# Kernel tuning notes

Measured on AMD Instinct MI355X. Metric: run time of the kernel, lower is better.

Reference implementation:

```python
import jax, jax.numpy as jnp
import numpy as np

N_NODES = 100000
N_EDGES = 1600000
IN_FEAT = 256
HIDDEN = 64
N_CLASSES = 16


def gcn_conv(x, edge_index, W, b):
    """PyG GCNConv: add self-loops, symmetric normalization, linear+aggregate."""
    n = x.shape[0]
    src, dst = edge_index[0], edge_index[1]
    loops = jnp.arange(n, dtype=src.dtype)
    src = jnp.concatenate([src, loops])
    dst = jnp.concatenate([dst, loops])
    # in-degree on graph with self-loops
    deg = jax.ops.segment_sum(jnp.ones(src.shape[0], dtype=x.dtype), dst, num_segments=n)
    dinv = jnp.where(deg > 0, jax.lax.rsqrt(deg), 0.0)
    h = x @ W                                  # [N, out]
    norm = dinv[src] * dinv[dst]               # [E+N]
    msg = h[src] * norm[:, None]                # gather + scale (memory-bound)
    out = jax.ops.segment_sum(msg, dst, num_segments=n)  # scatter-add
    return out + b


def setup_inputs() -> dict:
    key = jax.random.key(0)
    ks = jax.random.split(key, 5)
    x = jax.random.normal(ks[0], (N_NODES, IN_FEAT), dtype=jnp.float32)
    edge_index = jax.random.randint(ks[1], (2, N_EDGES), 0, N_NODES, dtype=jnp.int64)
    W1 = jax.random.normal(ks[2], (IN_FEAT, HIDDEN), dtype=jnp.float32) * (1.0 / np.sqrt(IN_FEAT))
    b1 = jnp.zeros((HIDDEN,), dtype=jnp.float32)
    W2 = jax.random.normal(ks[3], (HIDDEN, N_CLASSES), dtype=jnp.float32) * (1.0 / np.sqrt(HIDDEN))
    b2 = jnp.zeros((N_CLASSES,), dtype=jnp.float32)
    return {"x": x, "edge_index": edge_index, "W1": W1, "b1": b1, "W2": W2, "b2": b2}


def reference(x, edge_index, W1, b1, W2, b2):
    h = gcn_conv(x, edge_index, W1, b1)
    h = jax.nn.relu(h)
    # dropout p=0.5 is identity in eval mode (training=False)
    out = gcn_conv(h, edge_index, W2, b2)
    return out
```

## Files before the change

### kernel.cpp

```cpp
#include <hip/hip_runtime.h>

#define NN 100000
#define NE 1600000
#define FIN 256
#define FH 64
#define FC 16

#define NPB 512
#define NBKT ((NN + NPB - 1) / NPB)
#define NBLK 256
#define CHUNK (NE / NBLK)
#define CAP 12288
#define NB_GEMM1 ((NN + 127) / 128)

typedef int v2i __attribute__((ext_vector_type(2)));
typedef int v4i __attribute__((ext_vector_type(4)));
typedef short s16x8 __attribute__((ext_vector_type(8)));
typedef float f32x4 __attribute__((ext_vector_type(4)));

__device__ __forceinline__ float4 fma4(float4 v, float w, float4 a) {
    a.x = fmaf(v.x, w, a.x); a.y = fmaf(v.y, w, a.y);
    a.z = fmaf(v.z, w, a.z); a.w = fmaf(v.w, w, a.w);
    return a;
}
__device__ __forceinline__ float4 add4(float4 a, float4 v) {
    a.x += v.x; a.y += v.y; a.z += v.z; a.w += v.w;
    return a;
}
__device__ __forceinline__ float4 xor_add4(float4 r, int m) {
    r.x += __shfl_xor(r.x, m, 64); r.y += __shfl_xor(r.y, m, 64);
    r.z += __shfl_xor(r.z, m, 64); r.w += __shfl_xor(r.w, m, 64);
    return r;
}

__device__ __forceinline__ unsigned short bf16rne(float f) {
    unsigned u = __float_as_uint(f);
    u += 0x7FFFu + ((u >> 16) & 1u);
    return (unsigned short)(u >> 16);
}
__device__ __forceinline__ void split8(const float* f, s16x8& hi, s16x8& lo) {
    #pragma unroll
    for (int i = 0; i < 8; i++) {
        unsigned u = __float_as_uint(f[i]);
        unsigned short h = (unsigned short)((u + 0x7FFFu + ((u >> 16) & 1u)) >> 16);
        float l = f[i] - __uint_as_float((unsigned)h << 16);
        unsigned ul = __float_as_uint(l);
        hi[i] = (short)h;
        lo[i] = (short)((ul + 0x7FFFu + ((ul >> 16) & 1u)) >> 16);
    }
}

__global__ __launch_bounds__(256) void prep_k(const int* __restrict__ ei,
                                              int* __restrict__ flag,
                                              const float* __restrict__ W,
                                              unsigned short* __restrict__ Whi,
                                              unsigned short* __restrict__ Wlo) {
    int b = blockIdx.x;
    if (b == 8) {
        if (threadIdx.x == 0) {
            int z = (ei[1] == 0) & (ei[3] == 0) & (ei[5] == 0) & (ei[7] == 0);
            *flag = z;
        }
        return;
    }
    int slot = b * 256 + threadIdx.x;
    int l = slot & 63;
    int c = (slot >> 6) & 3;
    int s = slot >> 8;
    int k0 = s * 32 + (l >> 4) * 8;
    int col = c * 16 + (l & 15);
    #pragma unroll
    for (int i = 0; i < 8; i++) {
        float f = W[(k0 + i) * FH + col];
        unsigned short h = bf16rne(f);
        float lres = f - __uint_as_float((unsigned)h << 16);
        Whi[slot * 8 + i] = h;
        Wlo[slot * 8 + i] = bf16rne(lres);
    }
}

__global__ __launch_bounds__(256, 4) void gemm1_k(const float* __restrict__ x,
                                                  const unsigned short* __restrict__ Whi,
                                                  const unsigned short* __restrict__ Wlo,
                                                  float* __restrict__ h1) {
    const int t = threadIdx.x;
    const int lane = t & 63;
    const int wid = t >> 6;
    const int mb = blockIdx.x * 128 + wid * 32;
    const int lr = lane & 15;
    const int lk = (lane >> 4) * 8;

    int ra0 = mb + lr;
    int ra1 = mb + 16 + lr;
    const float* pa0 = x + (size_t)(ra0 < NN ? ra0 : NN - 1) * FIN + lk;
    const float* pa1 = x + (size_t)(ra1 < NN ? ra1 : NN - 1) * FIN + lk;

    f32x4 acc[2][4] = {};

    for (int s = 0; s < 8; s++) {
        float fa0[8], fa1[8];
        float4 q;
        q = *(const float4*)(pa0 + s * 32);
        fa0[0] = q.x; fa0[1] = q.y; fa0[2] = q.z; fa0[3] = q.w;
        q = *(const float4*)(pa0 + s * 32 + 4);
        fa0[4] = q.x; fa0[5] = q.y; fa0[6] = q.z; fa0[7] = q.w;
        q = *(const float4*)(pa1 + s * 32);
        fa1[0] = q.x; fa1[1] = q.y; fa1[2] = q.z; fa1[3] = q.w;
        q = *(const float4*)(pa1 + s * 32 + 4);
        fa1[4] = q.x; fa1[5] = q.y; fa1[6] = q.z; fa1[7] = q.w;

        s16x8 a0h, a0l, a1h, a1l;
        split8(fa0, a0h, a0l);
        split8(fa1, a1h, a1l);

        #pragma unroll
        for (int c = 0; c < 4; c++) {
            s16x8 wh = *(const s16x8*)&Whi[((s * 4 + c) * 64 + lane) * 8];
            s16x8 wl = *(const s16x8*)&Wlo[((s * 4 + c) * 64 + lane) * 8];
            acc[0][c] = __builtin_amdgcn_mfma_f32_16x16x32_bf16(a0h, wh, acc[0][c], 0, 0, 0);
            acc[0][c] = __builtin_amdgcn_mfma_f32_16x16x32_bf16(a0l, wh, acc[0][c], 0, 0, 0);
            acc[0][c] = __builtin_amdgcn_mfma_f32_16x16x32_bf16(a0h, wl, acc[0][c], 0, 0, 0);
            acc[1][c] = __builtin_amdgcn_mfma_f32_16x16x32_bf16(a1h, wh, acc[1][c], 0, 0, 0);
            acc[1][c] = __builtin_amdgcn_mfma_f32_16x16x32_bf16(a1l, wh, acc[1][c], 0, 0, 0);
            acc[1][c] = __builtin_amdgcn_mfma_f32_16x16x32_bf16(a1h, wl, acc[1][c], 0, 0, 0);
        }
    }
    #pragma unroll
    for (int r = 0; r < 2; r++) {
        int rowb = mb + 16 * r + (lane >> 4) * 4;
        #pragma unroll
        for (int c = 0; c < 4; c++) {
            #pragma unroll
            for (int v = 0; v < 4; v++) {
                int row = rowb + v;
                if (row < NN)
                    h1[(size_t)row * FH + 16 * c + lr] = acc[r][c][v];
            }
        }
    }
}

__global__ __launch_bounds__(256) void hist_k(const int* __restrict__ ei,
                                              const int* __restrict__ flag,
                                              int* __restrict__ cnt) {
    __shared__ int hist[NBKT];
    const int t = threadIdx.x, blk = blockIdx.x;
    for (int j = t; j < NBKT; j += 256) hist[j] = 0;
    __syncthreads();
    int f = *flag;
    int base = blk * CHUNK;
    if (f) {
        for (int i = t; i < CHUNK; i += 256) {
            v2i p = *(const v2i*)&ei[2 * (NE + base + i)];
            atomicAdd(&hist[p.x >> 9], 1);
        }
    } else {
        for (int i = t; i < CHUNK; i += 256) {
            int d = ei[NE + base + i];
            atomicAdd(&hist[d >> 9], 1);
        }
    }
    __syncthreads();
    for (int j = t; j < NBKT; j += 256) cnt[j * NBLK + blk] = hist[j];
}

__global__ __launch_bounds__(1024) void scanoff_k(int* __restrict__ cnt,
                                                  int* __restrict__ bucketBase) {
    __shared__ int s[1024];
    const int t = threadIdx.x;
    const int SEG = (NBKT * NBLK) / 1024;
    int base = t * SEG;
    int sum = 0;
    for (int i = 0; i < SEG; i++) sum += cnt[base + i];
    s[t] = sum; __syncthreads();
    for (int off = 1; off < 1024; off <<= 1) {
        int u = (t >= off) ? s[t - off] : 0;
        __syncthreads();
        s[t] += u;
        __syncthreads();
    }
    int run = s[t] - sum;
    for (int i = 0; i < SEG; i++) {
        int g = base + i;
        int v = cnt[g];
        cnt[g] = run;
        if ((g & (NBLK - 1)) == 0) bucketBase[g / NBLK] = run;
        run += v;
    }
    if (t == 0) bucketBase[NBKT] = NE;
}

__global__ __launch_bounds__(256) void scat_k(const int* __restrict__ ei,
                                              const int* __restrict__ flag,
                                              const int* __restrict__ cnt,
                                              int* __restrict__ sorted) {
    __shared__ int offl[NBKT];
    const int t = threadIdx.x, blk = blockIdx.x;
    for (int j = t; j < NBKT; j += 256) offl[j] = cnt[j * NBLK + blk];
    __syncthreads();
    int f = *flag;
    int base = blk * CHUNK;
    if (f) {
        for (int i = t; i < CHUNK; i += 256) {
            int e = base + i;
            v2i ps = *(const v2i*)&ei[2 * e];
            v2i pd = *(const v2i*)&ei[2 * (NE + e)];
            int s = ps.x, d = pd.x;
            int pos = atomicAdd(&offl[d >> 9], 1);
            sorted[pos] = s | ((d & (NPB - 1)) << 17);
        }
    } else {
        for (int i = t; i < CHUNK; i += 256) {
            int e = base + i;
            int s = ei[e], d = ei[NE + e];
            int pos = atomicAdd(&offl[d >> 9], 1);
            sorted[pos] = s | ((d & (NPB - 1)) << 17);
        }
    }
}

__global__ __launch_bounds__(256) void bucket_k(const int* __restrict__ sorted,
                                                const int* __restrict__ bucketBase,
                                                int* __restrict__ csr,
                                                int* __restrict__ row_start,
                                                float* __restrict__ dinv,
                                                float* __restrict__ h1) {
    __shared__ int stash[CAP];
    __shared__ int hist[NPB];
    __shared__ int startl[NPB];
    __shared__ int cursor[NPB];
    __shared__ int ss[256];
    const int t = threadIdx.x, b = blockIdx.x;
    const int nb0 = b * NPB;
    const int ncnt = (NN - nb0 < NPB) ? (NN - nb0) : NPB;
    const int ebase = bucketBase[b];
    const int ecnt = bucketBase[b + 1] - ebase;

    hist[t] = 0; hist[t + 256] = 0;
    __syncthreads();
    for (int i = t; i < ecnt; i += 256) {
        int v = sorted[ebase + i];
        if (i < CAP) stash[i] = v;
        atomicAdd(&hist[v >> 17], 1);
    }
    __syncthreads();
    int a = hist[2 * t], c = hist[2 * t + 1];
    int p = a + c;
    ss[t] = p; __syncthreads();
    for (int off = 1; off < 256; off <<= 1) {
        int u = (t >= off) ? ss[t - off] : 0;
        __syncthreads();
        ss[t] += u;
        __syncthreads();
    }
    int ex = ss[t] - p;
    startl[2 * t] = ex;       startl[2 * t + 1] = ex + a;
    cursor[2 * t] = ex;       cursor[2 * t + 1] = ex + a;
    __syncthreads();
    for (int j = t; j < ncnt; j += 256) {
        row_start[nb0 + j] = ebase + startl[j];
        dinv[nb0 + j] = rsqrtf((float)(hist[j] + 1));
    }
    if (b == 0 && t == 0) row_start[NN] = NE;
    for (int i = t; i < ecnt; i += 256) {
        int v = (i < CAP) ? stash[i] : sorted[ebase + i];
        int dl = v >> 17;
        int r = atomicAdd(&cursor[dl], 1);
        csr[ebase + r] = v & 0x1FFFF;
    }
    for (int q = t; q < ncnt * 16; q += 256) {
        int rl = q >> 4;
        float dv = rsqrtf((float)(hist[rl] + 1));
        size_t off = (size_t)(nb0 + rl) * FH + (q & 15) * 4;
        float4 v = *(const float4*)&h1[off];
        v.x *= dv; v.y *= dv; v.z *= dv; v.w *= dv;
        *(float4*)&h1[off] = v;
    }
}

__global__ __launch_bounds__(256) void agg1g_k(const int* __restrict__ csr,
                                               const int* __restrict__ row_start,
                                               const float* __restrict__ h1,
                                               const float* __restrict__ dinv,
                                               const float* __restrict__ b1,
                                               const float* __restrict__ W2,
                                               float* __restrict__ h2) {
    __shared__ float sW2[FH * FC];
    __shared__ float sp[4][FH];
    const int t = threadIdx.x;
    #pragma unroll
    for (int i = 0; i < 4; i++) sW2[t + 256 * i] = W2[t + 256 * i];
    __syncthreads();

    int wid = t >> 6;
    int n = blockIdx.x * 4 + wid;
    int lane = t & 63;
    if (n >= NN) return;
    int sg = lane >> 4;
    int fl = lane & 15;
    int s0 = row_start[n], s1 = row_start[n + 1];
    float4 A = make_float4(0.f, 0.f, 0.f, 0.f);
    float4 B = make_float4(0.f, 0.f, 0.f, 0.f);
    float4 C = make_float4(0.f, 0.f, 0.f, 0.f);
    float4 D = make_float4(0.f, 0.f, 0.f, 0.f);
    for (int j0 = s0; j0 < s1; j0 += 64) {
        int idx = j0 + lane;
        int sl = (idx < s1) ? csr[idx] : 0;
        int cnt = s1 - j0; if (cnt > 64) cnt = 64;
        int j = 0;
        for (; j + 16 <= cnt; j += 16) {
            int eA = __shfl(sl, j + sg, 64);
            int eB = __shfl(sl, j + 4 + sg, 64);
            int eC = __shfl(sl, j + 8 + sg, 64);
            int eD = __shfl(sl, j + 12 + sg, 64);
            float4 vA = *(const float4*)&h1[eA * FH + fl * 4];
            float4 vB = *(const float4*)&h1[eB * FH + fl * 4];
            float4 vC = *(const float4*)&h1[eC * FH + fl * 4];
            float4 vD = *(const float4*)&h1[eD * FH + fl * 4];
            A = add4(A, vA); B = add4(B, vB);
            C = add4(C, vC); D = add4(D, vD);
        }
        if (j + 8 <= cnt) {
            int eA = __shfl(sl, j + sg, 64);
            int eB = __shfl(sl, j + 4 + sg, 64);
            float4 vA = *(const float4*)&h1[eA * FH + fl * 4];
            float4 vB = *(const float4*)&h1[eB * FH + fl * 4];
            A = add4(A, vA); B = add4(B, vB);
            j += 8;
        }
        if (j + 4 <= cnt) {
            int eA = __shfl(sl, j + sg, 64);
            float4 vA = *(const float4*)&h1[eA * FH + fl * 4];
            A = add4(A, vA);
            j += 4;
        }
        int rem = cnt - j;
        if (rem > 0) {
            int jj = j + (sg < rem ? sg : 0);
            int eA = __shfl(sl, jj, 64);
            float wA = (sg < rem) ? 1.f : 0.f;
            float4 vA = *(const float4*)&h1[eA * FH + fl * 4];
            A = fma4(vA, wA, A);
        }
    }
    float4 r = add4(add4(A, B), add4(C, D));
    r = xor_add4(r, 16);
    r = xor_add4(r, 32);
    float dn = dinv[n];
    if (sg == 0) {
        float4 self = *(const float4*)&h1[n * FH + fl * 4];
        float4 bq = *(const float4*)&b1[fl * 4];
        float4 p;
        p.x = fmaxf(fmaf(r.x + self.x, dn, bq.x), 0.f);
        p.y = fmaxf(fmaf(r.y + self.y, dn, bq.y), 0.f);
        p.z = fmaxf(fmaf(r.z + self.z, dn, bq.z), 0.f);
        p.w = fmaxf(fmaf(r.w + self.w, dn, bq.w), 0.f);
        *(float4*)&sp[wid][fl * 4] = p;
    }
    __builtin_amdgcn_s_waitcnt(0);
    if (lane < FC) {
        float o = 0.f;
        #pragma unroll 8
        for (int k = 0; k < FH; k++)
            o = fmaf(sp[wid][k], sW2[k * FC + lane], o);
        h2[n * FC + lane] = o * dn;
    }
}

__global__ __launch_bounds__(256) void agg2_k(const int* __restrict__ csr,
                                              const int* __restrict__ row_start,
                                              const float* __restrict__ h2,
                                              const float* __restrict__ dinv,
                                              const float* __restrict__ b2,
                                              float* __restrict__ out) {
    const int t = threadIdx.x;
    int n = blockIdx.x * 16 + (t >> 4);
    int l16 = t & 15;
    int base = t & 48;
    int q = (t >> 2) & 3;
    int c = t & 3;
    if (n >= NN) return;
    int s0 = row_start[n], s1 = row_start[n + 1];
    float4 A = make_float4(0.f, 0.f, 0.f, 0.f);
    float4 B = make_float4(0.f, 0.f, 0.f, 0.f);
    float4 C = make_float4(0.f, 0.f, 0.f, 0.f);
    float4 D = make_float4(0.f, 0.f, 0.f, 0.f);
    for (int j0 = s0; j0 < s1; j0 += 16) {
        int idx = j0 + l16;
        int sl = (idx < s1) ? csr[idx] : 0;
        int cnt = s1 - j0; if (cnt > 16) cnt = 16;
        int j = 0;
        if (j + 16 <= cnt) {
            int eA = __shfl(sl, base + j + q, 64);
            int eB = __shfl(sl, base + j + 4 + q, 64);
            int eC = __shfl(sl, base + j + 8 + q, 64);
            int eD = __shfl(sl, base + j + 12 + q, 64);
            float4 vA = *(const float4*)&h2[eA * FC + c * 4];
            float4 vB = *(const float4*)&h2[eB * FC + c * 4];
            float4 vC = *(const float4*)&h2[eC * FC + c * 4];
            float4 vD = *(const float4*)&h2[eD * FC + c * 4];
            A = add4(A, vA); B = add4(B, vB);
            C = add4(C, vC); D = add4(D, vD);
            j += 16;
        }
        if (j + 8 <= cnt) {
            int eA = __shfl(sl, base + j + q, 64);
            int eB = __shfl(sl, base + j + 4 + q, 64);
            float4 vA = *(const float4*)&h2[eA * FC + c * 4];
            float4 vB = *(const float4*)&h2[eB * FC + c * 4];
            A = add4(A, vA); B = add4(B, vB);
            j += 8;
        }
        if (j + 4 <= cnt) {
            int eA = __shfl(sl, base + j + q, 64);
            float4 vA = *(const float4*)&h2[eA * FC + c * 4];
            A = add4(A, vA);
            j += 4;
        }
        int rem = cnt - j;
        if (rem > 0) {
            int jj = base + j + (q < rem ? q : 0);
            int eA = __shfl(sl, jj, 64);
            float wA = (q < rem) ? 1.f : 0.f;
            float4 vA = *(const float4*)&h2[eA * FC + c * 4];
            A = fma4(vA, wA, A);
        }
    }
    float4 r = add4(add4(A, B), add4(C, D));
    r = xor_add4(r, 4);
    r = xor_add4(r, 8);
    if (q == 0) {
        float dn = dinv[n];
        float4 self = *(const float4*)&h2[n * FC + c * 4];
        float4 bq = *(const float4*)&b2[c * 4];
        float4 p;
        p.x = fmaf(r.x + self.x, dn, bq.x);
        p.y = fmaf(r.y + self.y, dn, bq.y);
        p.z = fmaf(r.z + self.z, dn, bq.z);
        p.w = fmaf(r.w + self.w, dn, bq.w);
        *(float4*)&out[n * FC + c * 4] = p;
    }
}

extern "C" void kernel_launch(void* const* d_in, const int* in_sizes, int n_in,
                              void* d_out, int out_size, void* d_ws, size_t ws_size,
                              hipStream_t stream) {
    const float* x  = (const float*)d_in[0];
    const int*   ei = (const int*)d_in[1];
    const float* W1 = (const float*)d_in[2];
    const float* b1 = (const float*)d_in[3];
    const float* W2 = (const float*)d_in[4];
    const float* b2 = (const float*)d_in[5];
    float* out = (float*)d_out;

    char* ws = (char*)d_ws;
    int*   row_start  = (int*)(ws + 0);
    float* dinv       = (float*)(ws + 512ull * 1024);
    int*   flag       = (int*)(ws + 1024ull * 1024);
    int*   bucketBase = (int*)(ws + 1028ull * 1024);
    unsigned short* Whi = (unsigned short*)(ws + 1040ull * 1024);
    unsigned short* Wlo = (unsigned short*)(ws + 1072ull * 1024);
    int*   cnt        = (int*)(ws + 1104ull * 1024);
    int*   csr        = (int*)(ws + 2048ull * 1024);
    int*   sorted     = (int*)(ws + 9216ull * 1024);
    float* h2         = (float*)(ws + 9216ull * 1024);
    float* h1         = (float*)(ws + 16384ull * 1024);

    prep_k<<<9, 256, 0, stream>>>(ei, flag, W1, Whi, Wlo);
    gemm1_k<<<NB_GEMM1, 256, 0, stream>>>(x, Whi, Wlo, h1);
    hist_k<<<NBLK, 256, 0, stream>>>(ei, flag, cnt);
    scanoff_k<<<1, 1024, 0, stream>>>(cnt, bucketBase);
    scat_k<<<NBLK, 256, 0, stream>>>(ei, flag, cnt, sorted);
    bucket_k<<<NBKT, 256, 0, stream>>>(sorted, bucketBase, csr, row_start, dinv, h1);

    agg1g_k<<<(NN + 3) / 4, 256, 0, stream>>>(csr, row_start, h1, dinv, b1, W2, h2);
    agg2_k<<<(NN + 15) / 16, 256, 0, stream>>>(csr, row_start, h2, dinv, b2, out);
}
```

Before: 398.2 us.

## Store gathered features in fp16, fold dinv scaling into GEMM epilogue, merge prep kernels

Intermediate node features h1 and h2 are now stored as fp16 instead of fp32, which halves the bytes moved by the random-gather aggregation kernels. GEMM1 now runs after the CSR build so it can apply the dinv row scaling in its epilogue. This removes the separate read-modify-write pass over h1 that bucket_k used to do. The weight-prep and histogram kernels are merged into one launch, and the index-width flag is recomputed inline instead of going through memory. The cost is fp16 rounding error on the features and a changed kernel order.

```diff
diff --git a/kernel.cpp b/kernel.cpp
--- a/kernel.cpp
+++ b/kernel.cpp
@@ -17,6 +17,8 @@
 typedef int v4i __attribute__((ext_vector_type(4)));
 typedef short s16x8 __attribute__((ext_vector_type(8)));
 typedef float f32x4 __attribute__((ext_vector_type(4)));
+typedef _Float16 h16x8 __attribute__((ext_vector_type(8)));
+typedef _Float16 h16x4 __attribute__((ext_vector_type(4)));
 
 __device__ __forceinline__ float4 fma4(float4 v, float w, float4 a) {
     a.x = fmaf(v.x, w, a.x); a.y = fmaf(v.y, w, a.y);
@@ -49,105 +51,38 @@
         lo[i] = (short)((ul + 0x7FFFu + ((ul >> 16) & 1u)) >> 16);
     }
 }
-
-__global__ __launch_bounds__(256) void prep_k(const int* __restrict__ ei,
-                                              int* __restrict__ flag,
-                                              const float* __restrict__ W,
-                                              unsigned short* __restrict__ Whi,
-                                              unsigned short* __restrict__ Wlo) {
-    int b = blockIdx.x;
-    if (b == 8) {
-        if (threadIdx.x == 0) {
-            int z = (ei[1] == 0) & (ei[3] == 0) & (ei[5] == 0) & (ei[7] == 0);
-            *flag = z;
+__device__ __forceinline__ int is64(const int* __restrict__ ei) {
+    return (ei[1] == 0) & (ei[3] == 0) & (ei[5] == 0) & (ei[7] == 0);
+}
+
+__global__ __launch_bounds__(256) void histprep_k(const int* __restrict__ ei,
+                                                  const float* __restrict__ W,
+                                                  unsigned short* __restrict__ Whi,
+                                                  unsigned short* __restrict__ Wlo,
+                                                  int* __restrict__ cnt) {
+    const int b = blockIdx.x, t = threadIdx.x;
+    if (b < 8) {
+        int slot = b * 256 + t;
+        int l = slot & 63;
+        int c = (slot >> 6) & 3;
+        int s = slot >> 8;
+        int k0 = s * 32 + (l >> 4) * 8;
+        int col = c * 16 + (l & 15);
+        #pragma unroll
+        for (int i = 0; i < 8; i++) {
+            float f = W[(k0 + i) * FH + col];
+            unsigned short h = bf16rne(f);
+            float lres = f - __uint_as_float((unsigned)h << 16);
+            Whi[slot * 8 + i] = h;
+            Wlo[slot * 8 + i] = bf16rne(lres);
         }
         return;
     }
-    int slot = b * 256 + threadIdx.x;
-    int l = slot & 63;
-    int c = (slot >> 6) & 3;
-    int s = slot >> 8;
-    int k0 = s * 32 + (l >> 4) * 8;
-    int col = c * 16 + (l & 15);
-    #pragma unroll
-    for (int i = 0; i < 8; i++) {
-        float f = W[(k0 + i) * FH + col];
-        unsigned short h = bf16rne(f);
-        float lres = f - __uint_as_float((unsigned)h << 16);
-        Whi[slot * 8 + i] = h;
-        Wlo[slot * 8 + i] = bf16rne(lres);
-    }
-}
-
-__global__ __launch_bounds__(256, 4) void gemm1_k(const float* __restrict__ x,
-                                                  const unsigned short* __restrict__ Whi,
-                                                  const unsigned short* __restrict__ Wlo,
-                                                  float* __restrict__ h1) {
-    const int t = threadIdx.x;
-    const int lane = t & 63;
-    const int wid = t >> 6;
-    const int mb = blockIdx.x * 128 + wid * 32;
-    const int lr = lane & 15;
-    const int lk = (lane >> 4) * 8;
-
-    int ra0 = mb + lr;
-    int ra1 = mb + 16 + lr;
-    const float* pa0 = x + (size_t)(ra0 < NN ? ra0 : NN - 1) * FIN + lk;
-    const float* pa1 = x + (size_t)(ra1 < NN ? ra1 : NN - 1) * FIN + lk;
-
-    f32x4 acc[2][4] = {};
-
-    for (int s = 0; s < 8; s++) {
-        float fa0[8], fa1[8];
-        float4 q;
-        q = *(const float4*)(pa0 + s * 32);
-        fa0[0] = q.x; fa0[1] = q.y; fa0[2] = q.z; fa0[3] = q.w;
-        q = *(const float4*)(pa0 + s * 32 + 4);
-        fa0[4] = q.x; fa0[5] = q.y; fa0[6] = q.z; fa0[7] = q.w;
-        q = *(const float4*)(pa1 + s * 32);
-        fa1[0] = q.x; fa1[1] = q.y; fa1[2] = q.z; fa1[3] = q.w;
-        q = *(const float4*)(pa1 + s * 32 + 4);
-        fa1[4] = q.x; fa1[5] = q.y; fa1[6] = q.z; fa1[7] = q.w;
-
-        s16x8 a0h, a0l, a1h, a1l;
-        split8(fa0, a0h, a0l);
-        split8(fa1, a1h, a1l);
-
-        #pragma unroll
-        for (int c = 0; c < 4; c++) {
-            s16x8 wh = *(const s16x8*)&Whi[((s * 4 + c) * 64 + lane) * 8];
-            s16x8 wl = *(const s16x8*)&Wlo[((s * 4 + c) * 64 + lane) * 8];
-            acc[0][c] = __builtin_amdgcn_mfma_f32_16x16x32_bf16(a0h, wh, acc[0][c], 0, 0, 0);
-            acc[0][c] = __builtin_amdgcn_mfma_f32_16x16x32_bf16(a0l, wh, acc[0][c], 0, 0, 0);
-            acc[0][c] = __builtin_amdgcn_mfma_f32_16x16x32_bf16(a0h, wl, acc[0][c], 0, 0, 0);
-            acc[1][c] = __builtin_amdgcn_mfma_f32_16x16x32_bf16(a1h, wh, acc[1][c], 0, 0, 0);
-            acc[1][c] = __builtin_amdgcn_mfma_f32_16x16x32_bf16(a1l, wh, acc[1][c], 0, 0, 0);
-            acc[1][c] = __builtin_amdgcn_mfma_f32_16x16x32_bf16(a1h, wl, acc[1][c], 0, 0, 0);
-        }
-    }
-    #pragma unroll
-    for (int r = 0; r < 2; r++) {
-        int rowb = mb + 16 * r + (lane >> 4) * 4;
-        #pragma unroll
-        for (int c = 0; c < 4; c++) {
-            #pragma unroll
-            for (int v = 0; v < 4; v++) {
-                int row = rowb + v;
-                if (row < NN)
-                    h1[(size_t)row * FH + 16 * c + lr] = acc[r][c][v];
-            }
-        }
-    }
-}
-
-__global__ __launch_bounds__(256) void hist_k(const int* __restrict__ ei,
-                                              const int* __restrict__ flag,
-                                              int* __restrict__ cnt) {
     __shared__ int hist[NBKT];
-    const int t = threadIdx.x, blk = blockIdx.x;
+    const int blk = b - 8;
     for (int j = t; j < NBKT; j += 256) hist[j] = 0;
     __syncthreads();
-    int f = *flag;
+    int f = is64(ei);
     int base = blk * CHUNK;
     if (f) {
         for (int i = t; i < CHUNK; i += 256) {
@@ -191,14 +126,13 @@
 }
 
 __global__ __launch_bounds__(256) void scat_k(const int* __restrict__ ei,
-                                              const int* __restrict__ flag,
                                               const int* __restrict__ cnt,
                                               int* __restrict__ sorted) {
     __shared__ int offl[NBKT];
     const int t = threadIdx.x, blk = blockIdx.x;
     for (int j = t; j < NBKT; j += 256) offl[j] = cnt[j * NBLK + blk];
     __syncthreads();
-    int f = *flag;
+    int f = is64(ei);
     int base = blk * CHUNK;
     if (f) {
         for (int i = t; i < CHUNK; i += 256) {
@@ -223,8 +157,7 @@
                                                 const int* __restrict__ bucketBase,
                                                 int* __restrict__ csr,
                                                 int* __restrict__ row_start,
-                                                float* __restrict__ dinv,
-                                                float* __restrict__ h1) {
+                                                float* __restrict__ dinv) {
     __shared__ int stash[CAP];
     __shared__ int hist[NPB];
     __shared__ int startl[NPB];
@@ -268,23 +201,78 @@
         int r = atomicAdd(&cursor[dl], 1);
         csr[ebase + r] = v & 0x1FFFF;
     }
-    for (int q = t; q < ncnt * 16; q += 256) {
-        int rl = q >> 4;
-        float dv = rsqrtf((float)(hist[rl] + 1));
-        size_t off = (size_t)(nb0 + rl) * FH + (q & 15) * 4;
-        float4 v = *(const float4*)&h1[off];
-        v.x *= dv; v.y *= dv; v.z *= dv; v.w *= dv;
-        *(float4*)&h1[off] = v;
+}
+
+__global__ __launch_bounds__(256, 4) void gemm1_k(const float* __restrict__ x,
+                                                  const unsigned short* __restrict__ Whi,
+                                                  const unsigned short* __restrict__ Wlo,
+                                                  const float* __restrict__ dinv,
+                                                  _Float16* __restrict__ h1h) {
+    const int t = threadIdx.x;
+    const int lane = t & 63;
+    const int wid = t >> 6;
+    const int mb = blockIdx.x * 128 + wid * 32;
+    const int lr = lane & 15;
+    const int lk = (lane >> 4) * 8;
+
+    int ra0 = mb + lr;
+    int ra1 = mb + 16 + lr;
+    const float* pa0 = x + (size_t)(ra0 < NN ? ra0 : NN - 1) * FIN + lk;
+    const float* pa1 = x + (size_t)(ra1 < NN ? ra1 : NN - 1) * FIN + lk;
+
+    f32x4 acc[2][4] = {};
+
+    for (int s = 0; s < 8; s++) {
+        float fa0[8], fa1[8];
+        float4 q;
+        q = *(const float4*)(pa0 + s * 32);
+        fa0[0] = q.x; fa0[1] = q.y; fa0[2] = q.z; fa0[3] = q.w;
+        q = *(const float4*)(pa0 + s * 32 + 4);
+        fa0[4] = q.x; fa0[5] = q.y; fa0[6] = q.z; fa0[7] = q.w;
+        q = *(const float4*)(pa1 + s * 32);
+        fa1[0] = q.x; fa1[1] = q.y; fa1[2] = q.z; fa1[3] = q.w;
+        q = *(const float4*)(pa1 + s * 32 + 4);
+        fa1[4] = q.x; fa1[5] = q.y; fa1[6] = q.z; fa1[7] = q.w;
+
+        s16x8 a0h, a0l, a1h, a1l;
+        split8(fa0, a0h, a0l);
+        split8(fa1, a1h, a1l);
+
+        #pragma unroll
+        for (int c = 0; c < 4; c++) {
+            s16x8 wh = *(const s16x8*)&Whi[((s * 4 + c) * 64 + lane) * 8];
+            s16x8 wl = *(const s16x8*)&Wlo[((s * 4 + c) * 64 + lane) * 8];
+            acc[0][c] = __builtin_amdgcn_mfma_f32_16x16x32_bf16(a0h, wh, acc[0][c], 0, 0, 0);
+            acc[0][c] = __builtin_amdgcn_mfma_f32_16x16x32_bf16(a0l, wh, acc[0][c], 0, 0, 0);
+            acc[0][c] = __builtin_amdgcn_mfma_f32_16x16x32_bf16(a0h, wl, acc[0][c], 0, 0, 0);
+            acc[1][c] = __builtin_amdgcn_mfma_f32_16x16x32_bf16(a1h, wh, acc[1][c], 0, 0, 0);
+            acc[1][c] = __builtin_amdgcn_mfma_f32_16x16x32_bf16(a1l, wh, acc[1][c], 0, 0, 0);
+            acc[1][c] = __builtin_amdgcn_mfma_f32_16x16x32_bf16(a1h, wl, acc[1][c], 0, 0, 0);
+        }
+    }
+    #pragma unroll
+    for (int r = 0; r < 2; r++) {
+        int rowb = mb + 16 * r + (lane >> 4) * 4;
+        #pragma unroll
+        for (int v = 0; v < 4; v++) {
+            int row = rowb + v;
+            if (row < NN) {
+                float dn = dinv[row];
+                #pragma unroll
+                for (int c = 0; c < 4; c++)
+                    h1h[(size_t)row * FH + 16 * c + lr] = (_Float16)(acc[r][c][v] * dn);
+            }
+        }
     }
 }
 
 __global__ __launch_bounds__(256) void agg1g_k(const int* __restrict__ csr,
                                                const int* __restrict__ row_start,
-                                               const float* __restrict__ h1,
+                                               const _Float16* __restrict__ h1h,
                                                const float* __restrict__ dinv,
                                                const float* __restrict__ b1,
                                                const float* __restrict__ W2,
-                                               float* __restrict__ h2) {
+                                               _Float16* __restrict__ h2h) {
     __shared__ float sW2[FH * FC];
     __shared__ float sp[4][FH];
     const int t = threadIdx.x;
@@ -292,17 +280,15 @@
     for (int i = 0; i < 4; i++) sW2[t + 256 * i] = W2[t + 256 * i];
     __syncthreads();
 
-    int wid = t >> 6;
-    int n = blockIdx.x * 4 + wid;
-    int lane = t & 63;
+    const int wid = t >> 6;
+    const int n = blockIdx.x * 4 + wid;
+    const int lane = t & 63;
     if (n >= NN) return;
-    int sg = lane >> 4;
-    int fl = lane & 15;
+    const int sg = lane >> 3;
+    const int fl = lane & 7;
+    const h16x8* hp = (const h16x8*)h1h;
     int s0 = row_start[n], s1 = row_start[n + 1];
-    float4 A = make_float4(0.f, 0.f, 0.f, 0.f);
-    float4 B = make_float4(0.f, 0.f, 0.f, 0.f);
-    float4 C = make_float4(0.f, 0.f, 0.f, 0.f);
-    float4 D = make_float4(0.f, 0.f, 0.f, 0.f);
+    float aA[8] = {}, aB[8] = {};
     for (int j0 = s0; j0 < s1; j0 += 64) {
         int idx = j0 + lane;
         int sl = (idx < s1) ? csr[idx] : 0;
@@ -310,52 +296,53 @@
         int j = 0;
         for (; j + 16 <= cnt; j += 16) {
             int eA = __shfl(sl, j + sg, 64);
-            int eB = __shfl(sl, j + 4 + sg, 64);
-            int eC = __shfl(sl, j + 8 + sg, 64);
-            int eD = __shfl(sl, j + 12 + sg, 64);
-            float4 vA = *(const float4*)&h1[eA * FH + fl * 4];
-            float4 vB = *(const float4*)&h1[eB * FH + fl * 4];
-            float4 vC = *(const float4*)&h1[eC * FH + fl * 4];
-            float4 vD = *(const float4*)&h1[eD * FH + fl * 4];
-            A = add4(A, vA); B = add4(B, vB);
-            C = add4(C, vC); D = add4(D, vD);
+            int eB = __shfl(sl, j + 8 + sg, 64);
+            h16x8 vA = hp[eA * 8 + fl];
+            h16x8 vB = hp[eB * 8 + fl];
+            #pragma unroll
+            for (int i = 0; i < 8; i++) { aA[i] += (float)vA[i]; aB[i] += (float)vB[i]; }
         }
         if (j + 8 <= cnt) {
             int eA = __shfl(sl, j + sg, 64);
-            int eB = __shfl(sl, j + 4 + sg, 64);
-            float4 vA = *(const float4*)&h1[eA * FH + fl * 4];
-            float4 vB = *(const float4*)&h1[eB * FH + fl * 4];
-            A = add4(A, vA); B = add4(B, vB);
+            h16x8 vA = hp[eA * 8 + fl];
+            #pragma unroll
+            for (int i = 0; i < 8; i++) aA[i] += (float)vA[i];
             j += 8;
-        }
-        if (j + 4 <= cnt) {
-            int eA = __shfl(sl, j + sg, 64);
-            float4 vA = *(const float4*)&h1[eA * FH + fl * 4];
-            A = add4(A, vA);
-            j += 4;
         }
         int rem = cnt - j;
         if (rem > 0) {
             int jj = j + (sg < rem ? sg : 0);
             int eA = __shfl(sl, jj, 64);
-            float wA = (sg < rem) ? 1.f : 0.f;
-            float4 vA = *(const float4*)&h1[eA * FH + fl * 4];
-            A = fma4(vA, wA, A);
-        }
-    }
-    float4 r = add4(add4(A, B), add4(C, D));
-    r = xor_add4(r, 16);
-    r = xor_add4(r, 32);
+            float w = (sg < rem) ? 1.f : 0.f;
+            h16x8 vA = hp[eA * 8 + fl];
+            #pragma unroll
+            for (int i = 0; i < 8; i++) aA[i] = fmaf(w, (float)vA[i], aA[i]);
+        }
+    }
+    #pragma unroll
+    for (int i = 0; i < 8; i++) {
+        float r = aA[i] + aB[i];
+        r += __shfl_xor(r, 8, 64);
+        r += __shfl_xor(r, 16, 64);
+        r += __shfl_xor(r, 32, 64);
+        aA[i] = r;
+    }
     float dn = dinv[n];
     if (sg == 0) {
-        float4 self = *(const float4*)&h1[n * FH + fl * 4];
-        float4 bq = *(const float4*)&b1[fl * 4];
-        float4 p;
-        p.x = fmaxf(fmaf(r.x + self.x, dn, bq.x), 0.f);
-        p.y = fmaxf(fmaf(r.y + self.y, dn, bq.y), 0.f);
-        p.z = fmaxf(fmaf(r.z + self.z, dn, bq.z), 0.f);
-        p.w = fmaxf(fmaf(r.w + self.w, dn, bq.w), 0.f);
-        *(float4*)&sp[wid][fl * 4] = p;
+        h16x8 sv = hp[n * 8 + fl];
+        float4 p0, p1;
+        float4 bq0 = *(const float4*)&b1[fl * 8];
+        float4 bq1 = *(const float4*)&b1[fl * 8 + 4];
+        p0.x = fmaxf(fmaf(aA[0] + (float)sv[0], dn, bq0.x), 0.f);
+        p0.y = fmaxf(fmaf(aA[1] + (float)sv[1], dn, bq0.y), 0.f);
+        p0.z = fmaxf(fmaf(aA[2] + (float)sv[2], dn, bq0.z), 0.f);
+        p0.w = fmaxf(fmaf(aA[3] + (float)sv[3], dn, bq0.w), 0.f);
+        p1.x = fmaxf(fmaf(aA[4] + (float)sv[4], dn, bq1.x), 0.f);
+        p1.y = fmaxf(fmaf(aA[5] + (float)sv[5], dn, bq1.y), 0.f);
+        p1.z = fmaxf(fmaf(aA[6] + (float)sv[6], dn, bq1.z), 0.f);
+        p1.w = fmaxf(fmaf(aA[7] + (float)sv[7], dn, bq1.w), 0.f);
+        *(float4*)&sp[wid][fl * 8] = p0;
+        *(float4*)&sp[wid][fl * 8 + 4] = p1;
     }
     __builtin_amdgcn_s_waitcnt(0);
     if (lane < FC) {
@@ -363,13 +350,13 @@
         #pragma unroll 8
         for (int k = 0; k < FH; k++)
             o = fmaf(sp[wid][k], sW2[k * FC + lane], o);
-        h2[n * FC + lane] = o * dn;
+        h2h[n * FC + lane] = (_Float16)(o * dn);
     }
 }
 
 __global__ __launch_bounds__(256) void agg2_k(const int* __restrict__ csr,
                                               const int* __restrict__ row_start,
-                                              const float* __restrict__ h2,
+                                              const _Float16* __restrict__ h2h,
                                               const float* __restrict__ dinv,
                                               const float* __restrict__ b2,
                                               float* __restrict__ out) {
@@ -380,6 +367,7 @@
     int q = (t >> 2) & 3;
     int c = t & 3;
     if (n >= NN) return;
+    const h16x4* hp = (const h16x4*)h2h;
     int s0 = row_start[n], s1 = row_start[n + 1];
     float4 A = make_float4(0.f, 0.f, 0.f, 0.f);
     float4 B = make_float4(0.f, 0.f, 0.f, 0.f);
@@ -395,26 +383,29 @@
             int eB = __shfl(sl, base + j + 4 + q, 64);
             int eC = __shfl(sl, base + j + 8 + q, 64);
             int eD = __shfl(sl, base + j + 12 + q, 64);
-            float4 vA = *(const float4*)&h2[eA * FC + c * 4];
-            float4 vB = *(const float4*)&h2[eB * FC + c * 4];
-            float4 vC = *(const float4*)&h2[eC * FC + c * 4];
-            float4 vD = *(const float4*)&h2[eD * FC + c * 4];
-            A = add4(A, vA); B = add4(B, vB);
-            C = add4(C, vC); D = add4(D, vD);
+            h16x4 vA = hp[eA * 4 + c];
+            h16x4 vB = hp[eB * 4 + c];
+            h16x4 vC = hp[eC * 4 + c];
+            h16x4 vD = hp[eD * 4 + c];
+            A.x += (float)vA[0]; A.y += (float)vA[1]; A.z += (float)vA[2]; A.w += (float)vA[3];
+            B.x += (float)vB[0]; B.y += (float)vB[1]; B.z += (float)vB[2]; B.w += (float)vB[3];
+            C.x += (float)vC[0]; C.y += (float)vC[1]; C.z += (float)vC[2]; C.w += (float)vC[3];
+            D.x += (float)vD[0]; D.y += (float)vD[1]; D.z += (float)vD[2]; D.w += (float)vD[3];
             j += 16;
         }
         if (j + 8 <= cnt) {
             int eA = __shfl(sl, base + j + q, 64);
             int eB = __shfl(sl, base + j + 4 + q, 64);
-            float4 vA = *(const float4*)&h2[eA * FC + c * 4];
-            float4 vB = *(const float4*)&h2[eB * FC + c * 4];
-            A = add4(A, vA); B = add4(B, vB);
+            h16x4 vA = hp[eA * 4 + c];
+            h16x4 vB = hp[eB * 4 + c];
+            A.x += (float)vA[0]; A.y += (float)vA[1]; A.z += (float)vA[2]; A.w += (float)vA[3];
+            B.x += (float)vB[0]; B.y += (float)vB[1]; B.z += (float)vB[2]; B.w += (float)vB[3];
             j += 8;
         }
         if (j + 4 <= cnt) {
             int eA = __shfl(sl, base + j + q, 64);
-            float4 vA = *(const float4*)&h2[eA * FC + c * 4];
-            A = add4(A, vA);
+            h16x4 vA = hp[eA * 4 + c];
+            A.x += (float)vA[0]; A.y += (float)vA[1]; A.z += (float)vA[2]; A.w += (float)vA[3];
             j += 4;
         }
         int rem = cnt - j;
@@ -422,8 +413,9 @@
             int jj = base + j + (q < rem ? q : 0);
             int eA = __shfl(sl, jj, 64);
             float wA = (q < rem) ? 1.f : 0.f;
-            float4 vA = *(const float4*)&h2[eA * FC + c * 4];
-            A = fma4(vA, wA, A);
+            h16x4 vA = hp[eA * 4 + c];
+            float4 vf = make_float4((float)vA[0], (float)vA[1], (float)vA[2], (float)vA[3]);
+            A = fma4(vf, wA, A);
         }
     }
     float4 r = add4(add4(A, B), add4(C, D));
@@ -431,13 +423,13 @@
     r = xor_add4(r, 8);
     if (q == 0) {
         float dn = dinv[n];
-        float4 self = *(const float4*)&h2[n * FC + c * 4];
+        h16x4 sv = hp[n * 4 + c];
         float4 bq = *(const float4*)&b2[c * 4];
         float4 p;
-        p.x = fmaf(r.x + self.x, dn, bq.x);
-        p.y = fmaf(r.y + self.y, dn, bq.y);
-        p.z = fmaf(r.z + self.z, dn, bq.z);
-        p.w = fmaf(r.w + self.w, dn, bq.w);
+        p.x = fmaf(r.x + (float)sv[0], dn, bq.x);
+        p.y = fmaf(r.y + (float)sv[1], dn, bq.y);
+        p.z = fmaf(r.z + (float)sv[2], dn, bq.z);
+        p.w = fmaf(r.w + (float)sv[3], dn, bq.w);
         *(float4*)&out[n * FC + c * 4] = p;
     }
 }
@@ -456,23 +448,20 @@
     char* ws = (char*)d_ws;
     int*   row_start  = (int*)(ws + 0);
     float* dinv       = (float*)(ws + 512ull * 1024);
-    int*   flag       = (int*)(ws + 1024ull * 1024);
-    int*   bucketBase = (int*)(ws + 1028ull * 1024);
-    unsigned short* Whi = (unsigned short*)(ws + 1040ull * 1024);
-    unsigned short* Wlo = (unsigned short*)(ws + 1072ull * 1024);
-    int*   cnt        = (int*)(ws + 1104ull * 1024);
+    int*   bucketBase = (int*)(ws + 960ull * 1024);
+    unsigned short* Whi = (unsigned short*)(ws + 1024ull * 1024);
+    unsigned short* Wlo = (unsigned short*)(ws + 1088ull * 1024);
+    int*   cnt        = (int*)(ws + 1152ull * 1024);
     int*   csr        = (int*)(ws + 2048ull * 1024);
     int*   sorted     = (int*)(ws + 9216ull * 1024);
-    float* h2         = (float*)(ws + 9216ull * 1024);
-    float* h1         = (float*)(ws + 16384ull * 1024);
-
-    prep_k<<<9, 256, 0, stream>>>(ei, flag, W1, Whi, Wlo);
-    gemm1_k<<<NB_GEMM1, 256, 0, stream>>>(x, Whi, Wlo, h1);
-    hist_k<<<NBLK, 256, 0, stream>>>(ei, flag, cnt);
+    _Float16* h1h     = (_Float16*)(ws + 16384ull * 1024);
+    _Float16* h2h     = (_Float16*)(ws + 30720ull * 1024);
+
+    histprep_k<<<8 + NBLK, 256, 0, stream>>>(ei, W1, Whi, Wlo, cnt);
     scanoff_k<<<1, 1024, 0, stream>>>(cnt, bucketBase);
-    scat_k<<<NBLK, 256, 0, stream>>>(ei, flag, cnt, sorted);
-    bucket_k<<<NBKT, 256, 0, stream>>>(sorted, bucketBase, csr, row_start, dinv, h1);
-
-    agg1g_k<<<(NN + 3) / 4, 256, 0, stream>>>(csr, row_start, h1, dinv, b1, W2, h2);
-    agg2_k<<<(NN + 15) / 16, 256, 0, stream>>>(csr, row_start, h2, dinv, b2, out);
-}
+    scat_k<<<NBLK, 256, 0, stream>>>(ei, cnt, sorted);
+    bucket_k<<<NBKT, 256, 0, stream>>>(sorted, bucketBase, csr, row_start, dinv);
+    gemm1_k<<<NB_GEMM1, 256, 0, stream>>>(x, Whi, Wlo, dinv, h1h);
+    agg1g_k<<<(NN + 3) / 4, 256, 0, stream>>>(csr, row_start, h1h, dinv, b1, W2, h2h);
+    agg2_k<<<(NN + 15) / 16, 256, 0, stream>>>(csr, row_start, h2h, dinv, b2, out);
+}
```

Measured after the change: 388.4 us. 2.5% less time.
